# Performance work log

Measured on AMD Instinct MI355X. Metric: run time of the kernel, lower is better.

## Reference

```python
import jax, jax.numpy as jnp
import numpy as np

EPS = 1e-5
THRESHOLD = 0.7   # ternary threshold factor
QMAX = 127.0      # 2**(act_bits-1) - 1 for act_bits=8


def setup_inputs() -> dict:
    key = jax.random.key(0)
    k1, k2 = jax.random.split(key)
    B, S, D_IN, D_OUT = 4, 8192, 1024, 1024
    x = jax.random.normal(k1, (B, S, D_IN), dtype=jnp.float32)
    weight = jax.random.normal(k2, (D_OUT, D_IN), dtype=jnp.float32) * np.sqrt(2.0 / D_IN)
    gamma = jnp.ones((D_IN,), dtype=jnp.float32)
    beta = jnp.zeros((D_IN,), dtype=jnp.float32)
    return {"x": x, "weight": weight, "gamma": gamma, "beta": beta}


def _fake_quant_act(x):
    # symmetric per-tensor int8 absmax fake quantization (dequantized)
    scale = jnp.maximum(jnp.max(jnp.abs(x)), 1e-8) / QMAX
    q = jnp.round(jnp.clip(x / scale, -QMAX, QMAX)) * scale
    return x + jax.lax.stop_gradient(q - x)  # STE


def _ternary_quant_weight(w):
    # BitNet W1.58: delta = threshold * mean|W|; alpha = mean|W| over kept entries
    absw = jnp.abs(w)
    delta = THRESHOLD * jnp.mean(absw)
    mask = (absw > delta).astype(w.dtype)
    alpha = jnp.sum(absw * mask) / jnp.maximum(jnp.sum(mask), 1.0)
    wq = alpha * jnp.sign(w) * mask
    return w + jax.lax.stop_gradient(wq - w)  # STE


def reference(x, weight, gamma, beta):
    # LayerNorm over last dim
    mu = jnp.mean(x, axis=-1, keepdims=True)
    var = jnp.mean(jnp.square(x - mu), axis=-1, keepdims=True)
    xn = (x - mu) * jax.lax.rsqrt(var + EPS) * gamma + beta
    xq = _fake_quant_act(xn)          # [B, S, D_in]
    wq = _ternary_quant_weight(weight)  # [D_out, D_in]
    return jnp.einsum('bsi,oi->bso', xq, wq)
```

## Files before the change

### kernel.cpp

```cpp
#include <hip/hip_runtime.h>
#include <hip/hip_bf16.h>


#define M_ROWS   32768
#define D_IN     1024
#define D_OUT    1024
#define W_ELEMS  (1024*1024)

typedef __attribute__((ext_vector_type(4))) int int4v;


__global__ __launch_bounds__(256) void ln_stats_kernel(
    const float* __restrict__ x, const float* __restrict__ gamma,
    const float* __restrict__ beta, float* __restrict__ mu_out,
    float* __restrict__ rstd_out, unsigned int* __restrict__ absmax_bits) {
  int t = threadIdx.x;
  int wave = t >> 6, lane = t & 63;
  int wgid = blockIdx.x * 4 + wave;

  float4 g[4], b[4];
  #pragma unroll
  for (int k = 0; k < 4; k++) {
    g[k] = ((const float4*)gamma)[lane + 64 * k];
    b[k] = ((const float4*)beta )[lane + 64 * k];
  }

  float amax = 0.0f;
  #pragma unroll 2
  for (int i = 0; i < 8; i++) {
    int row = wgid + 4096 * i;
    const float4* xr = (const float4*)(x + (size_t)row * D_IN);
    float4 v[4];
    #pragma unroll
    for (int k = 0; k < 4; k++) v[k] = xr[lane + 64 * k];
    float s = 0.0f, sq = 0.0f;
    #pragma unroll
    for (int k = 0; k < 4; k++) {
      s  += v[k].x + v[k].y + v[k].z + v[k].w;
      sq += v[k].x*v[k].x + v[k].y*v[k].y + v[k].z*v[k].z + v[k].w*v[k].w;
    }
    #pragma unroll
    for (int off = 1; off < 64; off <<= 1) {
      s  += __shfl_xor(s,  off, 64);
      sq += __shfl_xor(sq, off, 64);
    }
    float mu   = s * (1.0f / D_IN);
    float var  = sq * (1.0f / D_IN) - mu * mu;
    float rstd = rsqrtf(var + 1e-5f);
    if (lane == 0) { mu_out[row] = mu; rstd_out[row] = rstd; }
    #pragma unroll
    for (int k = 0; k < 4; k++) {
      float nx = (v[k].x - mu) * rstd * g[k].x + b[k].x;
      float ny = (v[k].y - mu) * rstd * g[k].y + b[k].y;
      float nz = (v[k].z - mu) * rstd * g[k].z + b[k].z;
      float nw = (v[k].w - mu) * rstd * g[k].w + b[k].w;
      amax = fmaxf(amax, fmaxf(fmaxf(fabsf(nx), fabsf(ny)),
                               fmaxf(fabsf(nz), fabsf(nw))));
    }
  }
  #pragma unroll
  for (int off = 1; off < 64; off <<= 1)
    amax = fmaxf(amax, __shfl_xor(amax, off, 64));
  __shared__ float wm[4];
  if (lane == 0) wm[wave] = amax;
  __syncthreads();
  if (t == 0) {
    float m = fmaxf(fmaxf(wm[0], wm[1]), fmaxf(wm[2], wm[3]));
    atomicMax(absmax_bits, __float_as_uint(m));
  }
}

__global__ __launch_bounds__(256) void w_sum_kernel(const float* __restrict__ w,
                                                    double* __restrict__ sumw) {
  int base = blockIdx.x * 1024 + threadIdx.x;
  double s = 0.0;
  #pragma unroll
  for (int j = 0; j < 4; j++) {
    float4 v = ((const float4*)w)[base + 256 * j];
    s += (double)fabsf(v.x) + (double)fabsf(v.y) +
         (double)fabsf(v.z) + (double)fabsf(v.w);
  }
  #pragma unroll
  for (int off = 1; off < 64; off <<= 1) s += __shfl_xor(s, off, 64);
  __shared__ double ls[4];
  int wave = threadIdx.x >> 6, lane = threadIdx.x & 63;
  if (lane == 0) ls[wave] = s;
  __syncthreads();
  if (threadIdx.x == 0) atomicAdd(sumw, ls[0] + ls[1] + ls[2] + ls[3]);
}

__global__ __launch_bounds__(256) void w_quant_kernel(
    const float* __restrict__ w, const double* __restrict__ sumw,
    signed char* __restrict__ qw, double* __restrict__ kept_sum,
    unsigned int* __restrict__ kept_cnt) {
  double delta = 0.7 * (*sumw) * (1.0 / (double)W_ELEMS);
  int base = blockIdx.x * 1024 + threadIdx.x;
  double ks = 0.0;
  int kc = 0;
  #pragma unroll
  for (int j = 0; j < 4; j++) {
    float4 v = ((const float4*)w)[base + 256 * j];
    char4 q;
    {
      double a = (double)fabsf(v.x); bool m = a > delta;
      q.x = m ? (v.x > 0.0f ? 1 : -1) : 0; if (m) { ks += a; kc++; }
    }
    {
      double a = (double)fabsf(v.y); bool m = a > delta;
      q.y = m ? (v.y > 0.0f ? 1 : -1) : 0; if (m) { ks += a; kc++; }
    }
    {
      double a = (double)fabsf(v.z); bool m = a > delta;
      q.z = m ? (v.z > 0.0f ? 1 : -1) : 0; if (m) { ks += a; kc++; }
    }
    {
      double a = (double)fabsf(v.w); bool m = a > delta;
      q.w = m ? (v.w > 0.0f ? 1 : -1) : 0; if (m) { ks += a; kc++; }
    }
    ((char4*)qw)[base + 256 * j] = q;
  }
  #pragma unroll
  for (int off = 1; off < 64; off <<= 1) {
    ks += __shfl_xor(ks, off, 64);
    kc += __shfl_xor(kc, off, 64);
  }
  __shared__ double lss[4];
  __shared__ int    lcc[4];
  int wave = threadIdx.x >> 6, lane = threadIdx.x & 63;
  if (lane == 0) { lss[wave] = ks; lcc[wave] = kc; }
  __syncthreads();
  if (threadIdx.x == 0) {
    atomicAdd(kept_sum, lss[0] + lss[1] + lss[2] + lss[3]);
    atomicAdd(kept_cnt, (unsigned int)(lcc[0] + lcc[1] + lcc[2] + lcc[3]));
  }
}

__global__ __launch_bounds__(256) void act_quant_kernel(
    const float* __restrict__ x, const float* __restrict__ gamma,
    const float* __restrict__ beta, const float* __restrict__ mu_arr,
    const float* __restrict__ rstd_arr,
    const unsigned int* __restrict__ absmax_bits, signed char* __restrict__ qx) {
  int t = threadIdx.x;
  float am = __uint_as_float(*absmax_bits);
  float scale = fmaxf(am, 1e-8f) / 127.0f;
  float4 g = ((const float4*)gamma)[t];
  float4 b = ((const float4*)beta)[t];
  #pragma unroll 2
  for (int i = 0; i < 16; i++) {
    int row = blockIdx.x * 16 + i;
    float mu = mu_arr[row], rstd = rstd_arr[row];
    float4 v = ((const float4*)(x + (size_t)row * D_IN))[t];
    float nx = ((v.x - mu) * rstd * g.x + b.x) / scale;
    float ny = ((v.y - mu) * rstd * g.y + b.y) / scale;
    float nz = ((v.z - mu) * rstd * g.z + b.z) / scale;
    float nw = ((v.w - mu) * rstd * g.w + b.w) / scale;
    char4 q;
    q.x = (signed char)(int)rintf(fminf(fmaxf(nx, -127.0f), 127.0f));
    q.y = (signed char)(int)rintf(fminf(fmaxf(ny, -127.0f), 127.0f));
    q.z = (signed char)(int)rintf(fminf(fmaxf(nz, -127.0f), 127.0f));
    q.w = (signed char)(int)rintf(fminf(fmaxf(nw, -127.0f), 127.0f));
    ((char4*)(qx + (size_t)row * D_IN))[t] = q;
  }
}

__device__ inline void async_copy16(const void* g, void* l) {
  __builtin_amdgcn_global_load_lds(
      (const __attribute__((address_space(1))) unsigned int*)g,
      (__attribute__((address_space(3))) unsigned int*)l, 16, 0, 0);
}

__global__ __launch_bounds__(256) void gemm_i8_kernel(
    const signed char* __restrict__ A,
    const signed char* __restrict__ B,
    float* __restrict__ C,
    const unsigned int* __restrict__ absmax_bits,
    const double* __restrict__ kept_sum, const unsigned int* __restrict__ kept_cnt) {
  __shared__ __align__(16) signed char sA[128 * 64];
  __shared__ __align__(16) signed char sB[128 * 64];
  int t = threadIdx.x;
  int wave = t >> 6, lane = t & 63;
  int m0 = blockIdx.y * 128;
  int n0 = blockIdx.x * 128;
  int wr = (wave >> 1) * 64;
  int wc = (wave & 1) * 64;

  int4v acc[4][4] = {};

  int row_st = t >> 2;
  int slot   = t & 3;
  int kg     = (slot - (row_st >> 1)) & 3;
  const signed char* Ag = A + (size_t)(m0 + row_st) * D_IN + kg * 16;
  const signed char* Bg = B + (size_t)(n0 + row_st) * D_IN + kg * 16;
  signed char* sAp = sA + t * 16;
  signed char* sBp = sB + t * 16;

  int lrow = lane & 15;
  int c    = lane >> 4;

  for (int k0 = 0; k0 < D_IN; k0 += 64) {
    async_copy16(Ag + k0, sAp);
    async_copy16(Ag + k0 + (size_t)64 * D_IN, sAp + 64 * 64);
    async_copy16(Bg + k0, sBp);
    async_copy16(Bg + k0 + (size_t)64 * D_IN, sBp + 64 * 64);
    __syncthreads();

    int4v af[4], bf[4];
    #pragma unroll
    for (int i = 0; i < 4; i++) {
      int r = wr + i * 16 + lrow;
      af[i] = *(const int4v*)(sA + r * 64 + (((c + (r >> 1)) & 3) * 16));
    }
    #pragma unroll
    for (int j = 0; j < 4; j++) {
      int r = wc + j * 16 + lrow;
      bf[j] = *(const int4v*)(sB + r * 64 + (((c + (r >> 1)) & 3) * 16));
    }
    #pragma unroll
    for (int i = 0; i < 4; i++)
      #pragma unroll
      for (int j = 0; j < 4; j++)
        acc[i][j] = __builtin_amdgcn_mfma_i32_16x16x64_i8(af[i], bf[j], acc[i][j], 0, 0, 0);
    __syncthreads();
  }

  float am = __uint_as_float(*absmax_bits);
  double alpha = (*kept_sum) / (double)max(*kept_cnt, 1u);
  float f = (float)(((double)fmaxf(am, 1e-8f) / 127.0) * alpha);

  int crow = m0 + wr + ((lane >> 4) << 2);
  int ccol = n0 + wc + (lane & 15);
  #pragma unroll
  for (int i = 0; i < 4; i++)
    #pragma unroll
    for (int j = 0; j < 4; j++)
      #pragma unroll
      for (int rr = 0; rr < 4; rr++) {
        int row = crow + i * 16 + rr;
        int col = ccol + j * 16;
        C[(size_t)row * D_OUT + col] = (float)acc[i][j][rr] * f;
      }
}

extern "C" void kernel_launch(void* const* d_in, const int* in_sizes, int n_in,
                              void* d_out, int out_size, void* d_ws, size_t ws_size,
                              hipStream_t stream) {
  const float* x     = (const float*)d_in[0];
  const float* w     = (const float*)d_in[1];
  const float* gamma = (const float*)d_in[2];
  const float* beta  = (const float*)d_in[3];
  float* out = (float*)d_out;

  char* ws = (char*)d_ws;
  unsigned int* absmax_bits = (unsigned int*)ws;
  unsigned int* kept_cnt    = (unsigned int*)(ws + 4);
  double* sumw     = (double*)(ws + 8);
  double* kept_sum = (double*)(ws + 16);
  float* mu   = (float*)(ws + 1024);
  float* rstd = (float*)(ws + 132096);
  signed char* qw = (signed char*)(ws + 263168);
  signed char* qx = (signed char*)(ws + 1311744);

  hipMemsetAsync(d_ws, 0, 64, stream);

  ln_stats_kernel<<<1024, 256, 0, stream>>>(x, gamma, beta, mu, rstd, absmax_bits);
  w_sum_kernel<<<256, 256, 0, stream>>>(w, sumw);
  w_quant_kernel<<<256, 256, 0, stream>>>(w, sumw, qw, kept_sum, kept_cnt);
  act_quant_kernel<<<2048, 256, 0, stream>>>(x, gamma, beta, mu, rstd, absmax_bits, qx);

  dim3 grid(D_OUT / 128, M_ROWS / 128);
  gemm_i8_kernel<<<grid, 256, 0, stream>>>(qx, qw, out, absmax_bits, kept_sum, kept_cnt);
}
```

Baseline: 320.0 us.

## Merge prep kernels and rewrite int8 GEMM with 256x256 double-buffered pipeline

Merges the LayerNorm-stats and weight-sum kernels, and the weight-quant and activation-quant kernels, into two combined launches. This cuts five launches to three and lets the independent work run concurrently. Replaces the 128x128 int8 GEMM with a 256x256-tile, 512-thread kernel that uses 128KB of dynamic LDS. That kernel double-buffers K=128 slices with async global-to-LDS loads, waits on explicit vmcnt/lgkmcnt counters, raises wave priority around MFMA blocks and remaps workgroups for L2 locality. The explicit waitcnt choreography is fragile, and the 128KB LDS request must be accepted by the launch.

```diff
diff --git a/kernel.cpp b/kernel.cpp
--- a/kernel.cpp
+++ b/kernel.cpp
@@ -10,234 +10,306 @@
 typedef __attribute__((ext_vector_type(4))) int int4v;
 
 
-__global__ __launch_bounds__(256) void ln_stats_kernel(
+__global__ __launch_bounds__(256) void ln_stats_wsum_kernel(
     const float* __restrict__ x, const float* __restrict__ gamma,
     const float* __restrict__ beta, float* __restrict__ mu_out,
-    float* __restrict__ rstd_out, unsigned int* __restrict__ absmax_bits) {
+    float* __restrict__ rstd_out, unsigned int* __restrict__ absmax_bits,
+    const float* __restrict__ w, double* __restrict__ sumw) {
+  __shared__ float wm[4];
+  __shared__ double ls[4];
   int t = threadIdx.x;
   int wave = t >> 6, lane = t & 63;
-  int wgid = blockIdx.x * 4 + wave;
-
-  float4 g[4], b[4];
-  #pragma unroll
-  for (int k = 0; k < 4; k++) {
-    g[k] = ((const float4*)gamma)[lane + 64 * k];
-    b[k] = ((const float4*)beta )[lane + 64 * k];
+
+  if (blockIdx.x < 1024) {
+    int wgid = blockIdx.x * 4 + wave;
+    float4 g[4], b[4];
+    #pragma unroll
+    for (int k = 0; k < 4; k++) {
+      g[k] = ((const float4*)gamma)[lane + 64 * k];
+      b[k] = ((const float4*)beta )[lane + 64 * k];
+    }
+    float amax = 0.0f;
+    #pragma unroll 2
+    for (int i = 0; i < 8; i++) {
+      int row = wgid + 4096 * i;
+      const float4* xr = (const float4*)(x + (size_t)row * D_IN);
+      float4 v[4];
+      #pragma unroll
+      for (int k = 0; k < 4; k++) v[k] = xr[lane + 64 * k];
+      float s = 0.0f, sq = 0.0f;
+      #pragma unroll
+      for (int k = 0; k < 4; k++) {
+        s  += v[k].x + v[k].y + v[k].z + v[k].w;
+        sq += v[k].x*v[k].x + v[k].y*v[k].y + v[k].z*v[k].z + v[k].w*v[k].w;
+      }
+      #pragma unroll
+      for (int off = 1; off < 64; off <<= 1) {
+        s  += __shfl_xor(s,  off, 64);
+        sq += __shfl_xor(sq, off, 64);
+      }
+      float mu   = s * (1.0f / D_IN);
+      float var  = sq * (1.0f / D_IN) - mu * mu;
+      float rstd = rsqrtf(var + 1e-5f);
+      if (lane == 0) { mu_out[row] = mu; rstd_out[row] = rstd; }
+      #pragma unroll
+      for (int k = 0; k < 4; k++) {
+        float nx = (v[k].x - mu) * rstd * g[k].x + b[k].x;
+        float ny = (v[k].y - mu) * rstd * g[k].y + b[k].y;
+        float nz = (v[k].z - mu) * rstd * g[k].z + b[k].z;
+        float nw = (v[k].w - mu) * rstd * g[k].w + b[k].w;
+        amax = fmaxf(amax, fmaxf(fmaxf(fabsf(nx), fabsf(ny)),
+                                 fmaxf(fabsf(nz), fabsf(nw))));
+      }
+    }
+    #pragma unroll
+    for (int off = 1; off < 64; off <<= 1)
+      amax = fmaxf(amax, __shfl_xor(amax, off, 64));
+    if (lane == 0) wm[wave] = amax;
+    __syncthreads();
+    if (t == 0) {
+      float m = fmaxf(fmaxf(wm[0], wm[1]), fmaxf(wm[2], wm[3]));
+      atomicMax(absmax_bits, __float_as_uint(m));
+    }
+  } else {
+    int base = (blockIdx.x - 1024) * 1024 + t;
+    double s = 0.0;
+    #pragma unroll
+    for (int j = 0; j < 4; j++) {
+      float4 v = ((const float4*)w)[base + 256 * j];
+      s += (double)fabsf(v.x) + (double)fabsf(v.y) +
+           (double)fabsf(v.z) + (double)fabsf(v.w);
+    }
+    #pragma unroll
+    for (int off = 1; off < 64; off <<= 1) s += __shfl_xor(s, off, 64);
+    if (lane == 0) ls[wave] = s;
+    __syncthreads();
+    if (t == 0) atomicAdd(sumw, ls[0] + ls[1] + ls[2] + ls[3]);
   }
-
-  float amax = 0.0f;
-  #pragma unroll 2
-  for (int i = 0; i < 8; i++) {
-    int row = wgid + 4096 * i;
-    const float4* xr = (const float4*)(x + (size_t)row * D_IN);
-    float4 v[4];
-    #pragma unroll
-    for (int k = 0; k < 4; k++) v[k] = xr[lane + 64 * k];
-    float s = 0.0f, sq = 0.0f;
-    #pragma unroll
-    for (int k = 0; k < 4; k++) {
-      s  += v[k].x + v[k].y + v[k].z + v[k].w;
-      sq += v[k].x*v[k].x + v[k].y*v[k].y + v[k].z*v[k].z + v[k].w*v[k].w;
-    }
-    #pragma unroll
-    for (int off = 1; off < 64; off <<= 1) {
-      s  += __shfl_xor(s,  off, 64);
-      sq += __shfl_xor(sq, off, 64);
-    }
-    float mu   = s * (1.0f / D_IN);
-    float var  = sq * (1.0f / D_IN) - mu * mu;
-    float rstd = rsqrtf(var + 1e-5f);
-    if (lane == 0) { mu_out[row] = mu; rstd_out[row] = rstd; }
-    #pragma unroll
-    for (int k = 0; k < 4; k++) {
-      float nx = (v[k].x - mu) * rstd * g[k].x + b[k].x;
-      float ny = (v[k].y - mu) * rstd * g[k].y + b[k].y;
-      float nz = (v[k].z - mu) * rstd * g[k].z + b[k].z;
-      float nw = (v[k].w - mu) * rstd * g[k].w + b[k].w;
-      amax = fmaxf(amax, fmaxf(fmaxf(fabsf(nx), fabsf(ny)),
-                               fmaxf(fabsf(nz), fabsf(nw))));
-    }
-  }
-  #pragma unroll
-  for (int off = 1; off < 64; off <<= 1)
-    amax = fmaxf(amax, __shfl_xor(amax, off, 64));
-  __shared__ float wm[4];
-  if (lane == 0) wm[wave] = amax;
-  __syncthreads();
-  if (t == 0) {
-    float m = fmaxf(fmaxf(wm[0], wm[1]), fmaxf(wm[2], wm[3]));
-    atomicMax(absmax_bits, __float_as_uint(m));
-  }
-}
-
-__global__ __launch_bounds__(256) void w_sum_kernel(const float* __restrict__ w,
-                                                    double* __restrict__ sumw) {
-  int base = blockIdx.x * 1024 + threadIdx.x;
-  double s = 0.0;
-  #pragma unroll
-  for (int j = 0; j < 4; j++) {
-    float4 v = ((const float4*)w)[base + 256 * j];
-    s += (double)fabsf(v.x) + (double)fabsf(v.y) +
-         (double)fabsf(v.z) + (double)fabsf(v.w);
-  }
-  #pragma unroll
-  for (int off = 1; off < 64; off <<= 1) s += __shfl_xor(s, off, 64);
-  __shared__ double ls[4];
-  int wave = threadIdx.x >> 6, lane = threadIdx.x & 63;
-  if (lane == 0) ls[wave] = s;
-  __syncthreads();
-  if (threadIdx.x == 0) atomicAdd(sumw, ls[0] + ls[1] + ls[2] + ls[3]);
-}
-
-__global__ __launch_bounds__(256) void w_quant_kernel(
+}
+
+__global__ __launch_bounds__(256) void wquant_actquant_kernel(
     const float* __restrict__ w, const double* __restrict__ sumw,
     signed char* __restrict__ qw, double* __restrict__ kept_sum,
-    unsigned int* __restrict__ kept_cnt) {
-  double delta = 0.7 * (*sumw) * (1.0 / (double)W_ELEMS);
-  int base = blockIdx.x * 1024 + threadIdx.x;
-  double ks = 0.0;
-  int kc = 0;
-  #pragma unroll
-  for (int j = 0; j < 4; j++) {
-    float4 v = ((const float4*)w)[base + 256 * j];
-    char4 q;
-    {
-      double a = (double)fabsf(v.x); bool m = a > delta;
-      q.x = m ? (v.x > 0.0f ? 1 : -1) : 0; if (m) { ks += a; kc++; }
-    }
-    {
-      double a = (double)fabsf(v.y); bool m = a > delta;
-      q.y = m ? (v.y > 0.0f ? 1 : -1) : 0; if (m) { ks += a; kc++; }
-    }
-    {
-      double a = (double)fabsf(v.z); bool m = a > delta;
-      q.z = m ? (v.z > 0.0f ? 1 : -1) : 0; if (m) { ks += a; kc++; }
-    }
-    {
-      double a = (double)fabsf(v.w); bool m = a > delta;
-      q.w = m ? (v.w > 0.0f ? 1 : -1) : 0; if (m) { ks += a; kc++; }
-    }
-    ((char4*)qw)[base + 256 * j] = q;
-  }
-  #pragma unroll
-  for (int off = 1; off < 64; off <<= 1) {
-    ks += __shfl_xor(ks, off, 64);
-    kc += __shfl_xor(kc, off, 64);
-  }
-  __shared__ double lss[4];
-  __shared__ int    lcc[4];
-  int wave = threadIdx.x >> 6, lane = threadIdx.x & 63;
-  if (lane == 0) { lss[wave] = ks; lcc[wave] = kc; }
-  __syncthreads();
-  if (threadIdx.x == 0) {
-    atomicAdd(kept_sum, lss[0] + lss[1] + lss[2] + lss[3]);
-    atomicAdd(kept_cnt, (unsigned int)(lcc[0] + lcc[1] + lcc[2] + lcc[3]));
-  }
-}
-
-__global__ __launch_bounds__(256) void act_quant_kernel(
+    unsigned int* __restrict__ kept_cnt,
     const float* __restrict__ x, const float* __restrict__ gamma,
     const float* __restrict__ beta, const float* __restrict__ mu_arr,
     const float* __restrict__ rstd_arr,
     const unsigned int* __restrict__ absmax_bits, signed char* __restrict__ qx) {
+  __shared__ double lss[4];
+  __shared__ int    lcc[4];
   int t = threadIdx.x;
-  float am = __uint_as_float(*absmax_bits);
-  float scale = fmaxf(am, 1e-8f) / 127.0f;
-  float4 g = ((const float4*)gamma)[t];
-  float4 b = ((const float4*)beta)[t];
-  #pragma unroll 2
-  for (int i = 0; i < 16; i++) {
-    int row = blockIdx.x * 16 + i;
-    float mu = mu_arr[row], rstd = rstd_arr[row];
-    float4 v = ((const float4*)(x + (size_t)row * D_IN))[t];
-    float nx = ((v.x - mu) * rstd * g.x + b.x) / scale;
-    float ny = ((v.y - mu) * rstd * g.y + b.y) / scale;
-    float nz = ((v.z - mu) * rstd * g.z + b.z) / scale;
-    float nw = ((v.w - mu) * rstd * g.w + b.w) / scale;
-    char4 q;
-    q.x = (signed char)(int)rintf(fminf(fmaxf(nx, -127.0f), 127.0f));
-    q.y = (signed char)(int)rintf(fminf(fmaxf(ny, -127.0f), 127.0f));
-    q.z = (signed char)(int)rintf(fminf(fmaxf(nz, -127.0f), 127.0f));
-    q.w = (signed char)(int)rintf(fminf(fmaxf(nw, -127.0f), 127.0f));
-    ((char4*)(qx + (size_t)row * D_IN))[t] = q;
+
+  if (blockIdx.x < 256) {
+    double delta = 0.7 * (*sumw) * (1.0 / (double)W_ELEMS);
+    int base = blockIdx.x * 1024 + t;
+    double ks = 0.0;
+    int kc = 0;
+    #pragma unroll
+    for (int j = 0; j < 4; j++) {
+      float4 v = ((const float4*)w)[base + 256 * j];
+      char4 q;
+      {
+        double a = (double)fabsf(v.x); bool m = a > delta;
+        q.x = m ? (v.x > 0.0f ? 1 : -1) : 0; if (m) { ks += a; kc++; }
+      }
+      {
+        double a = (double)fabsf(v.y); bool m = a > delta;
+        q.y = m ? (v.y > 0.0f ? 1 : -1) : 0; if (m) { ks += a; kc++; }
+      }
+      {
+        double a = (double)fabsf(v.z); bool m = a > delta;
+        q.z = m ? (v.z > 0.0f ? 1 : -1) : 0; if (m) { ks += a; kc++; }
+      }
+      {
+        double a = (double)fabsf(v.w); bool m = a > delta;
+        q.w = m ? (v.w > 0.0f ? 1 : -1) : 0; if (m) { ks += a; kc++; }
+      }
+      ((char4*)qw)[base + 256 * j] = q;
+    }
+    #pragma unroll
+    for (int off = 1; off < 64; off <<= 1) {
+      ks += __shfl_xor(ks, off, 64);
+      kc += __shfl_xor(kc, off, 64);
+    }
+    int wave = t >> 6, lane = t & 63;
+    if (lane == 0) { lss[wave] = ks; lcc[wave] = kc; }
+    __syncthreads();
+    if (t == 0) {
+      atomicAdd(kept_sum, lss[0] + lss[1] + lss[2] + lss[3]);
+      atomicAdd(kept_cnt, (unsigned int)(lcc[0] + lcc[1] + lcc[2] + lcc[3]));
+    }
+  } else {
+    float am = __uint_as_float(*absmax_bits);
+    float scale = fmaxf(am, 1e-8f) / 127.0f;
+    float4 g = ((const float4*)gamma)[t];
+    float4 b = ((const float4*)beta)[t];
+    int bid2 = blockIdx.x - 256;
+    #pragma unroll 2
+    for (int i = 0; i < 16; i++) {
+      int row = bid2 * 16 + i;
+      float mu = mu_arr[row], rstd = rstd_arr[row];
+      float4 v = ((const float4*)(x + (size_t)row * D_IN))[t];
+      float nx = ((v.x - mu) * rstd * g.x + b.x) / scale;
+      float ny = ((v.y - mu) * rstd * g.y + b.y) / scale;
+      float nz = ((v.z - mu) * rstd * g.z + b.z) / scale;
+      float nw = ((v.w - mu) * rstd * g.w + b.w) / scale;
+      char4 q;
+      q.x = (signed char)(int)rintf(fminf(fmaxf(nx, -127.0f), 127.0f));
+      q.y = (signed char)(int)rintf(fminf(fmaxf(ny, -127.0f), 127.0f));
+      q.z = (signed char)(int)rintf(fminf(fmaxf(nz, -127.0f), 127.0f));
+      q.w = (signed char)(int)rintf(fminf(fmaxf(nw, -127.0f), 127.0f));
+      ((char4*)(qx + (size_t)row * D_IN))[t] = q;
+    }
   }
 }
 
-__device__ inline void async_copy16(const void* g, void* l) {
+
+__device__ __forceinline__ void stage16(const signed char* src, signed char* dst) {
   __builtin_amdgcn_global_load_lds(
-      (const __attribute__((address_space(1))) unsigned int*)g,
-      (__attribute__((address_space(3))) unsigned int*)l, 16, 0, 0);
-}
-
-__global__ __launch_bounds__(256) void gemm_i8_kernel(
+      (const __attribute__((address_space(1))) unsigned int*)src,
+      (__attribute__((address_space(3))) unsigned int*)dst, 16, 0, 0);
+}
+
+#define BAR()   __builtin_amdgcn_s_barrier()
+#define BARS()  { __builtin_amdgcn_s_barrier(); __builtin_amdgcn_sched_barrier(0); }
+#define LGKM0() { asm volatile("s_waitcnt lgkmcnt(0)" ::: "memory"); __builtin_amdgcn_sched_barrier(0); }
+#define VMW(N)  { asm volatile("s_waitcnt vmcnt(" #N ")" ::: "memory"); __builtin_amdgcn_sched_barrier(0); }
+
+#define STAGE_A(BUF, HALF, KB) { \
+  signed char* d_ = ldsA + (((BUF)*2 + (HALF)) << 14) + (tid << 4); \
+  const signed char* s_ = Asrc + (size_t)(HALF) * (128 * D_IN) + (KB); \
+  stage16(s_, d_); stage16(s_ + 64 * D_IN, d_ + 8192); }
+
+#define STAGE_B(BUF, HALF, KB) { \
+  signed char* d_ = ldsB + (((BUF)*2 + (HALF)) << 14) + (tid << 4); \
+  const signed char* s_ = Bsrc + (size_t)(HALF) * (128 * D_IN) + (KB); \
+  stage16(s_, d_); stage16(s_ + 64 * D_IN, d_ + 8192); }
+
+#define LOAD_A(P, RH) { _Pragma("unroll") \
+  for (int f_ = 0; f_ < 4; f_++) { \
+    const signed char* rp_ = (P) + (((RH)*64 + f_*16 + lrow) << 7); \
+    a[f_][0] = *(const int4v*)(rp_ + kA0); \
+    a[f_][1] = *(const int4v*)(rp_ + kA1); } }
+
+#define LOAD_B(P, CH) { _Pragma("unroll") \
+  for (int g_ = 0; g_ < 2; g_++) { \
+    const signed char* rp_ = (P) + ((bro + (CH)*32 + g_*16 + lrow) << 7); \
+    b[CH][g_][0] = *(const int4v*)(rp_ + kA0); \
+    b[CH][g_][1] = *(const int4v*)(rp_ + kA1); } }
+
+#define MFMA_Q(RH, CH) { _Pragma("unroll") \
+  for (int f_ = 0; f_ < 4; f_++) { _Pragma("unroll") \
+    for (int g_ = 0; g_ < 2; g_++) { \
+      acc[(RH)*4+f_][(CH)*2+g_] = __builtin_amdgcn_mfma_i32_16x16x64_i8( \
+          a[f_][0], b[CH][g_][0], acc[(RH)*4+f_][(CH)*2+g_], 0, 0, 0); \
+      acc[(RH)*4+f_][(CH)*2+g_] = __builtin_amdgcn_mfma_i32_16x16x64_i8( \
+          a[f_][1], b[CH][g_][1], acc[(RH)*4+f_][(CH)*2+g_], 0, 0, 0); } } }
+
+#define KITER(FULL, koO, koE2, koO2) \
+   \
+  LOAD_A(pA0, 0); LOAD_B(pB0, 0); \
+  STAGE_B(1, 1, koO); STAGE_A(1, 1, koO); \
+  asm volatile("s_waitcnt lgkmcnt(8)" ::: "memory"); \
+  BAR(); LGKM0(); \
+  __builtin_amdgcn_s_setprio(1); MFMA_Q(0, 0); __builtin_amdgcn_s_setprio(0); BARS(); \
+   \
+  LOAD_B(pB0, 1); BAR(); LGKM0(); \
+  __builtin_amdgcn_s_setprio(1); MFMA_Q(0, 1); __builtin_amdgcn_s_setprio(0); BARS(); \
+   \
+  LOAD_A(pA0, 1); if (FULL) { STAGE_B(0, 0, koE2); } BAR(); LGKM0(); \
+  __builtin_amdgcn_s_setprio(1); MFMA_Q(1, 0); __builtin_amdgcn_s_setprio(0); BARS(); \
+   \
+  if (FULL) { STAGE_B(0, 1, koE2); STAGE_A(0, 0, koE2); } BAR(); \
+  __builtin_amdgcn_s_setprio(1); MFMA_Q(1, 1); __builtin_amdgcn_s_setprio(0); \
+  if (FULL) { VMW(6); } else { VMW(0); } BARS(); \
+   \
+  LOAD_A(pA1, 0); LOAD_B(pB1, 0); if (FULL) { STAGE_A(0, 1, koE2); } \
+  asm volatile("s_waitcnt lgkmcnt(8)" ::: "memory"); \
+  BAR(); LGKM0(); \
+  __builtin_amdgcn_s_setprio(1); MFMA_Q(0, 0); __builtin_amdgcn_s_setprio(0); BARS(); \
+   \
+  LOAD_B(pB1, 1); BAR(); LGKM0(); \
+  __builtin_amdgcn_s_setprio(1); MFMA_Q(0, 1); __builtin_amdgcn_s_setprio(0); BARS(); \
+   \
+  LOAD_A(pA1, 1); if (FULL) { STAGE_B(1, 0, koO2); } BAR(); LGKM0(); \
+  __builtin_amdgcn_s_setprio(1); MFMA_Q(1, 0); __builtin_amdgcn_s_setprio(0); BARS(); \
+   \
+  if (FULL) { STAGE_A(1, 0, koO2); } BAR(); \
+  __builtin_amdgcn_s_setprio(1); MFMA_Q(1, 1); __builtin_amdgcn_s_setprio(0); \
+  if (FULL) { VMW(4); } BARS();
+
+__global__ __launch_bounds__(512, 2) void gemm_i8_256_kernel(
     const signed char* __restrict__ A,
     const signed char* __restrict__ B,
     float* __restrict__ C,
     const unsigned int* __restrict__ absmax_bits,
     const double* __restrict__ kept_sum, const unsigned int* __restrict__ kept_cnt) {
-  __shared__ __align__(16) signed char sA[128 * 64];
-  __shared__ __align__(16) signed char sB[128 * 64];
-  int t = threadIdx.x;
-  int wave = t >> 6, lane = t & 63;
-  int m0 = blockIdx.y * 128;
-  int n0 = blockIdx.x * 128;
-  int wr = (wave >> 1) * 64;
-  int wc = (wave & 1) * 64;
-
-  int4v acc[4][4] = {};
-
-  int row_st = t >> 2;
-  int slot   = t & 3;
-  int kg     = (slot - (row_st >> 1)) & 3;
-  const signed char* Ag = A + (size_t)(m0 + row_st) * D_IN + kg * 16;
-  const signed char* Bg = B + (size_t)(n0 + row_st) * D_IN + kg * 16;
-  signed char* sAp = sA + t * 16;
-  signed char* sBp = sB + t * 16;
-
-  int lrow = lane & 15;
-  int c    = lane >> 4;
-
-  for (int k0 = 0; k0 < D_IN; k0 += 64) {
-    async_copy16(Ag + k0, sAp);
-    async_copy16(Ag + k0 + (size_t)64 * D_IN, sAp + 64 * 64);
-    async_copy16(Bg + k0, sBp);
-    async_copy16(Bg + k0 + (size_t)64 * D_IN, sBp + 64 * 64);
-    __syncthreads();
-
-    int4v af[4], bf[4];
-    #pragma unroll
-    for (int i = 0; i < 4; i++) {
-      int r = wr + i * 16 + lrow;
-      af[i] = *(const int4v*)(sA + r * 64 + (((c + (r >> 1)) & 3) * 16));
-    }
-    #pragma unroll
-    for (int j = 0; j < 4; j++) {
-      int r = wc + j * 16 + lrow;
-      bf[j] = *(const int4v*)(sB + r * 64 + (((c + (r >> 1)) & 3) * 16));
-    }
-    #pragma unroll
-    for (int i = 0; i < 4; i++)
-      #pragma unroll
-      for (int j = 0; j < 4; j++)
-        acc[i][j] = __builtin_amdgcn_mfma_i32_16x16x64_i8(af[i], bf[j], acc[i][j], 0, 0, 0);
-    __syncthreads();
+  extern __shared__ __align__(16) signed char lds[];
+  signed char* ldsA = lds;
+  signed char* ldsB = lds + 65536;
+
+  const int tid = threadIdx.x;
+  const int lane = tid & 63;
+  const int wid = tid >> 6;
+  const int wr = wid >> 2;
+  const int wc = wid & 3;
+
+  int wg = ((blockIdx.x & 7) << 6) + (blockIdx.x >> 3);
+  const int m0 = (wg >> 2) << 8;
+  const int n0 = (wg & 3) << 8;
+
+  float am = __uint_as_float(*absmax_bits);
+  double ksum = *kept_sum;
+  unsigned int kcnt = *kept_cnt;
+  asm volatile("s_waitcnt vmcnt(0) lgkmcnt(0)" ::: "memory");
+  __builtin_amdgcn_sched_barrier(0);
+  double alpha = ksum / (double)max(kcnt, 1u);
+  float fscale = (float)(((double)fmaxf(am, 1e-8f) / 127.0) * alpha);
+
+  int so = (tid << 4) ^ (((tid >> 5) & 1) << 5);
+  int r0 = so >> 7, c0 = so & 127;
+  const signed char* Asrc = A + (size_t)(m0 + r0) * D_IN + c0;
+  const signed char* Bsrc = B + (size_t)(n0 + r0) * D_IN + c0;
+
+  const int lrow = lane & 15;
+  const int kA0 = ((lane >> 4) << 4) ^ (((lrow >> 2) & 1) << 5);
+  const int kA1 = 64 + kA0;
+  const int bro = (wc & 1) << 6;
+  const signed char* pA0 = ldsA + (wr << 14);
+  const signed char* pA1 = pA0 + 32768;
+  const signed char* pB0 = ldsB + ((wc >> 1) << 14);
+  const signed char* pB1 = pB0 + 32768;
+
+  int4v acc[8][4] = {};
+  int4v a[4][2];
+  int4v b[2][2][2];
+
+  STAGE_B(0, 0, 0); STAGE_B(0, 1, 0);
+  STAGE_A(0, 0, 0); STAGE_A(0, 1, 0);
+  STAGE_B(1, 0, 128); STAGE_A(1, 0, 128);
+  VMW(4); BARS();
+
+  for (int i = 0; i < 3; i++) {
+    int koO  = (2 * i + 1) * 128;
+    int koE2 = (2 * i + 2) * 128;
+    int koO2 = (2 * i + 3) * 128;
+    KITER(1, koO, koE2, koO2)
   }
-
-  float am = __uint_as_float(*absmax_bits);
-  double alpha = (*kept_sum) / (double)max(*kept_cnt, 1u);
-  float f = (float)(((double)fmaxf(am, 1e-8f) / 127.0) * alpha);
-
-  int crow = m0 + wr + ((lane >> 4) << 2);
-  int ccol = n0 + wc + (lane & 15);
+  {
+    int koO = 7 * 128;
+    KITER(0, koO, 0, 0)
+  }
+
+  const int crow0 = m0 + (wr << 7) + ((lane >> 4) << 2);
+  const int ccol0 = n0 + (wc << 6) + (lane & 15);
   #pragma unroll
-  for (int i = 0; i < 4; i++)
-    #pragma unroll
-    for (int j = 0; j < 4; j++)
+  for (int rf = 0; rf < 8; rf++)
+    #pragma unroll
+    for (int cf = 0; cf < 4; cf++)
       #pragma unroll
       for (int rr = 0; rr < 4; rr++) {
-        int row = crow + i * 16 + rr;
-        int col = ccol + j * 16;
-        C[(size_t)row * D_OUT + col] = (float)acc[i][j][rr] * f;
+        int row = crow0 + rf * 16 + rr;
+        C[(size_t)row * D_OUT + ccol0 + cf * 16] = (float)acc[rf][cf][rr] * fscale;
       }
 }
 
@@ -262,11 +334,11 @@
 
   hipMemsetAsync(d_ws, 0, 64, stream);
 
-  ln_stats_kernel<<<1024, 256, 0, stream>>>(x, gamma, beta, mu, rstd, absmax_bits);
-  w_sum_kernel<<<256, 256, 0, stream>>>(w, sumw);
-  w_quant_kernel<<<256, 256, 0, stream>>>(w, sumw, qw, kept_sum, kept_cnt);
-  act_quant_kernel<<<2048, 256, 0, stream>>>(x, gamma, beta, mu, rstd, absmax_bits, qx);
-
-  dim3 grid(D_OUT / 128, M_ROWS / 128);
-  gemm_i8_kernel<<<grid, 256, 0, stream>>>(qx, qw, out, absmax_bits, kept_sum, kept_cnt);
-}
+  ln_stats_wsum_kernel<<<1280, 256, 0, stream>>>(x, gamma, beta, mu, rstd,
+                                                 absmax_bits, w, sumw);
+  wquant_actquant_kernel<<<2304, 256, 0, stream>>>(w, sumw, qw, kept_sum, kept_cnt,
+                                                   x, gamma, beta, mu, rstd,
+                                                   absmax_bits, qx);
+  gemm_i8_256_kernel<<<512, 512, 131072, stream>>>(qx, qw, out, absmax_bits,
+                                                   kept_sum, kept_cnt);
+}
```

Result: faster. 301.6 us (-5.8%).
